# Performance work log

Measured on AMD Instinct MI355X. Metric: run time of the kernel, lower is better.

The kernel has to match this reference:

```python
import jax, jax.numpy as jnp
import numpy as np


def setup_inputs() -> dict:
    key = jax.random.key(0)
    kq, kk, kv = jax.random.split(key, 3)
    B, H, N, D = 4, 16, 2048, 64
    q = jax.random.normal(kq, (B, H, N, D), dtype=jnp.float32)
    k = jax.random.normal(kk, (B, N, D), dtype=jnp.float32)
    v = jax.random.normal(kv, (B, N, D), dtype=jnp.float32)
    return {"q": q, "k": k, "v": v}


def reference(q, k, v):
    # q: [B,H,N,D], k/v: [B,N,D] (KV shared across heads)
    scale = q.shape[-1] ** -0.5
    sim = jnp.einsum('bhid,bjd->bhij', q, k) * scale  # [B,H,N,N]
    attn = jax.nn.softmax(sim, axis=-1)
    return jnp.einsum('bhij,bjd->bhid', attn, v)  # [B,H,N,D]
```

## Files before the change

### kernel.cpp

```cpp
#include <hip/hip_runtime.h>
#include <hip/hip_bf16.h>

#define B_ 4
#define H_ 16
#define N_ 2048
#define D_ 64
#define BM 256
#define BN 64

typedef __bf16 bf16;
typedef bf16 bf16x4 __attribute__((ext_vector_type(4)));
typedef bf16 bf16x8 __attribute__((ext_vector_type(8)));
typedef float f32x2 __attribute__((ext_vector_type(2)));
typedef float f32x16 __attribute__((ext_vector_type(16)));

#define SCALE_LOG2E 0.18033688011112042f

#define GBL(p) ((const __attribute__((address_space(1))) void*)(p))
#define LDS(p) ((__attribute__((address_space(3))) void*)(p))

__global__ __launch_bounds__(256) void convert_kv(const float* __restrict__ k,
                                                  const float* __restrict__ v,
                                                  bf16* __restrict__ img) {
    const int tile = blockIdx.x >> 1;
    const int b = tile >> 5, T = tile & 31;
    const int pu = (blockIdx.x & 1) * 256 + threadIdx.x;
    const int mtks = pu >> 6;
    const int ln   = pu & 63;
    const int mt = mtks >> 2, ks = mtks & 3;
    bf16* timg = img + (size_t)tile * 8192;

    {
        const int kvr = T * 64 + mt * 32 + (ln & 31);
        const int d0  = ks * 16 + (ln >> 5) * 8;
        const float* src = k + ((size_t)b * N_ + kvr) * D_ + d0;
        float4 a = *(const float4*)src;
        float4 c = *(const float4*)(src + 4);
        bf16x8 o;
        o[0] = (bf16)a.x; o[1] = (bf16)a.y; o[2] = (bf16)a.z; o[3] = (bf16)a.w;
        o[4] = (bf16)c.x; o[5] = (bf16)c.y; o[6] = (bf16)c.z; o[7] = (bf16)c.w;
        *(bf16x8*)(timg + pu * 8) = o;
    }
    {
        const int d   = mt * 32 + (ln & 31);
        const int kv0 = T * 64 + ks * 16 + (ln >> 5) * 8;
        const float* src = v + ((size_t)b * N_ + kv0) * D_ + d;
        bf16x8 o;
        #pragma unroll
        for (int j = 0; j < 8; ++j) o[j] = (bf16)src[(size_t)j * D_];
        *(bf16x8*)(timg + 4096 + pu * 8) = o;
    }
}

static __device__ inline bf16x4 pack4(float a, float b, float c, float d) {
    bf16x4 r; r[0] = (bf16)a; r[1] = (bf16)b; r[2] = (bf16)c; r[3] = (bf16)d; return r;
}
static __device__ inline bf16x4 xor32(bf16x4 x) {
    f32x2 f = __builtin_bit_cast(f32x2, x);
    f32x2 g;
    g[0] = __shfl_xor(f[0], 32);
    g[1] = __shfl_xor(f[1], 32);
    return __builtin_bit_cast(bf16x4, g);
}

__global__ __launch_bounds__(256, 2) void attn_fwd(const float* __restrict__ q,
                                                   const bf16* __restrict__ img,
                                                   float* __restrict__ out) {
    __shared__ __align__(16) bf16 KV[2][8192];

    const int tid  = threadIdx.x;
    const int lane = tid & 63;
    const int wv   = tid >> 6;
    const int half = lane >> 5;
    const int l31  = lane & 31;

    const int bh = blockIdx.y;
    const int b  = bh >> 4;
    const int q0 = blockIdx.x * BM + wv * 64;

    const bf16* tiles = img + (size_t)b * 32 * 8192;

    bf16x8 qf[2][4];
    #pragma unroll
    for (int qn = 0; qn < 2; ++qn)
        #pragma unroll
        for (int ks = 0; ks < 4; ++ks) {
            const float* src = q + ((size_t)bh * N_ + q0 + qn * 32 + l31) * D_ + ks * 16 + half * 8;
            float4 a = *(const float4*)src;
            float4 c = *(const float4*)(src + 4);
            bf16x8 pk;
            pk[0] = (bf16)(a.x * SCALE_LOG2E); pk[1] = (bf16)(a.y * SCALE_LOG2E);
            pk[2] = (bf16)(a.z * SCALE_LOG2E); pk[3] = (bf16)(a.w * SCALE_LOG2E);
            pk[4] = (bf16)(c.x * SCALE_LOG2E); pk[5] = (bf16)(c.y * SCALE_LOG2E);
            pk[6] = (bf16)(c.z * SCALE_LOG2E); pk[7] = (bf16)(c.w * SCALE_LOG2E);
            qf[qn][ks] = pk;
        }

    f32x16 acc[2][2] = {{{}, {}}, {{}, {}}};
    float lacc[2] = {0.f, 0.f};

    auto issue_dma = [&](int it, int p) {
        const bf16* g = tiles + (size_t)it * 8192;
        #pragma unroll
        for (int j = 0; j < 4; ++j) {
            const int c = wv * 4 + j;
            __builtin_amdgcn_global_load_lds(GBL(g + c * 512 + lane * 8),
                                             LDS(&KV[p][c * 512]), 16, 0, 0);
        }
    };

    issue_dma(0, 0);

    for (int it = 0; it < N_ / BN; ++it) {
        const int p = it & 1;
        __syncthreads();
        if (it + 1 < N_ / BN) issue_dma(it + 1, p ^ 1);

        bf16x8 kf[2][4], vf[2][4];
        #pragma unroll
        for (int mt = 0; mt < 2; ++mt)
            #pragma unroll
            for (int ks = 0; ks < 4; ++ks) {
                kf[mt][ks] = *(const bf16x8*)&KV[p][((mt * 4 + ks) * 64 + lane) * 8];
                vf[mt][ks] = *(const bf16x8*)&KV[p][4096 + ((mt * 4 + ks) * 64 + lane) * 8];
            }

        #pragma unroll
        for (int qn = 0; qn < 2; ++qn) {
            f32x16 s[2] = {{}, {}};
            #pragma unroll
            for (int ks = 0; ks < 4; ++ks) {
                s[0] = __builtin_amdgcn_mfma_f32_32x32x16_bf16(kf[0][ks], qf[qn][ks], s[0], 0, 0, 0);
                s[1] = __builtin_amdgcn_mfma_f32_32x32x16_bf16(kf[1][ks], qf[qn][ks], s[1], 0, 0, 0);
            }
            #pragma unroll
            for (int mt = 0; mt < 2; ++mt) {
                float pv[16];
                #pragma unroll
                for (int r = 0; r < 16; ++r) pv[r] = __builtin_amdgcn_exp2f(s[mt][r]);
                float t0 = 0.f, t1 = 0.f;
                #pragma unroll
                for (int r = 0; r < 8; ++r) { t0 += pv[r]; t1 += pv[8 + r]; }
                lacc[qn] += t0 + t1;
                #pragma unroll
                for (int sp = 0; sp < 2; ++sp) {
                    bf16x4 lo  = pack4(pv[8 * sp + 0], pv[8 * sp + 1], pv[8 * sp + 2], pv[8 * sp + 3]);
                    bf16x4 hi  = pack4(pv[8 * sp + 4], pv[8 * sp + 5], pv[8 * sp + 6], pv[8 * sp + 7]);
                    bf16x4 xlo = xor32(lo), xhi = xor32(hi);
                    bf16x4 a0 = half ? xhi : lo;
                    bf16x4 a1 = half ? hi  : xlo;
                    bf16x8 bfrag = __builtin_shufflevector(a0, a1, 0, 1, 2, 3, 4, 5, 6, 7);
                    const int g = mt * 2 + sp;
                    acc[0][qn] = __builtin_amdgcn_mfma_f32_32x32x16_bf16(vf[0][g], bfrag, acc[0][qn], 0, 0, 0);
                    acc[1][qn] = __builtin_amdgcn_mfma_f32_32x32x16_bf16(vf[1][g], bfrag, acc[1][qn], 0, 0, 0);
                }
            }
        }
    }

    #pragma unroll
    for (int qn = 0; qn < 2; ++qn) {
        float l = lacc[qn] + __shfl_xor(lacc[qn], 32);
        float inv = 1.0f / l;
        const int qrow = q0 + qn * 32 + l31;
        float* dst = out + ((size_t)bh * N_ + qrow) * D_ + 4 * half;
        #pragma unroll
        for (int mt = 0; mt < 2; ++mt)
            #pragma unroll
            for (int rq = 0; rq < 4; ++rq) {
                float4 o;
                o.x = acc[mt][qn][4 * rq + 0] * inv;
                o.y = acc[mt][qn][4 * rq + 1] * inv;
                o.z = acc[mt][qn][4 * rq + 2] * inv;
                o.w = acc[mt][qn][4 * rq + 3] * inv;
                *(float4*)(dst + mt * 32 + 8 * rq) = o;
            }
    }
}

extern "C" void kernel_launch(void* const* d_in, const int* in_sizes, int n_in,
                              void* d_out, int out_size, void* d_ws, size_t ws_size,
                              hipStream_t stream) {
    const float* q = (const float*)d_in[0];
    const float* k = (const float*)d_in[1];
    const float* v = (const float*)d_in[2];
    float* out = (float*)d_out;

    bf16* img = (bf16*)d_ws;

    convert_kv<<<B_ * 64, 256, 0, stream>>>(k, v, img);
    dim3 grid(N_ / BM, B_ * H_);
    attn_fwd<<<grid, 256, 0, stream>>>(q, img, out);
}
```

Baseline: 155.3 us.

## Load K/V fragments directly from global into registers with double buffering

Drops the LDS staging buffer, the global_load_lds DMA and the per-iteration block barrier. Each wave now reads its K/V MFMA fragments straight from the pre-swizzled global image into two register sets, loading the next tile while computing the current one. The P-fragment cross-half exchange also changes from two shuffles to one shuffle of a selected half. This raises register pressure (two fragment sets) and makes every wave fetch the tile on its own through L2/L1 instead of sharing one LDS copy, which may hurt occupancy under launch_bounds(256,2).

```diff
diff --git a/kernel.cpp b/kernel.cpp
--- a/kernel.cpp
+++ b/kernel.cpp
@@ -15,9 +15,6 @@
 typedef float f32x16 __attribute__((ext_vector_type(16)));
 
 #define SCALE_LOG2E 0.18033688011112042f
-
-#define GBL(p) ((const __attribute__((address_space(1))) void*)(p))
-#define LDS(p) ((__attribute__((address_space(3))) void*)(p))
 
 __global__ __launch_bounds__(256) void convert_kv(const float* __restrict__ k,
                                                   const float* __restrict__ v,
@@ -55,7 +52,7 @@
 static __device__ inline bf16x4 pack4(float a, float b, float c, float d) {
     bf16x4 r; r[0] = (bf16)a; r[1] = (bf16)b; r[2] = (bf16)c; r[3] = (bf16)d; return r;
 }
-static __device__ inline bf16x4 xor32(bf16x4 x) {
+static __device__ inline bf16x4 xchg32(bf16x4 x) {
     f32x2 f = __builtin_bit_cast(f32x2, x);
     f32x2 g;
     g[0] = __shfl_xor(f[0], 32);
@@ -66,8 +63,6 @@
 __global__ __launch_bounds__(256, 2) void attn_fwd(const float* __restrict__ q,
                                                    const bf16* __restrict__ img,
                                                    float* __restrict__ out) {
-    __shared__ __align__(16) bf16 KV[2][8192];
-
     const int tid  = threadIdx.x;
     const int lane = tid & 63;
     const int wv   = tid >> 6;
@@ -78,7 +73,7 @@
     const int b  = bh >> 4;
     const int q0 = blockIdx.x * BM + wv * 64;
 
-    const bf16* tiles = img + (size_t)b * 32 * 8192;
+    const bf16* tb = img + (size_t)b * 32 * 8192 + lane * 8;
 
     bf16x8 qf[2][4];
     #pragma unroll
@@ -99,32 +94,18 @@
     f32x16 acc[2][2] = {{{}, {}}, {{}, {}}};
     float lacc[2] = {0.f, 0.f};
 
-    auto issue_dma = [&](int it, int p) {
-        const bf16* g = tiles + (size_t)it * 8192;
-        #pragma unroll
-        for (int j = 0; j < 4; ++j) {
-            const int c = wv * 4 + j;
-            __builtin_amdgcn_global_load_lds(GBL(g + c * 512 + lane * 8),
-                                             LDS(&KV[p][c * 512]), 16, 0, 0);
-        }
-    };
-
-    issue_dma(0, 0);
-
-    for (int it = 0; it < N_ / BN; ++it) {
-        const int p = it & 1;
-        __syncthreads();
-        if (it + 1 < N_ / BN) issue_dma(it + 1, p ^ 1);
-
-        bf16x8 kf[2][4], vf[2][4];
+    auto load_frags = [&](int it, bf16x8 (&kf)[2][4], bf16x8 (&vf)[2][4]) {
+        const bf16* g = tb + (size_t)it * 8192;
         #pragma unroll
         for (int mt = 0; mt < 2; ++mt)
             #pragma unroll
             for (int ks = 0; ks < 4; ++ks) {
-                kf[mt][ks] = *(const bf16x8*)&KV[p][((mt * 4 + ks) * 64 + lane) * 8];
-                vf[mt][ks] = *(const bf16x8*)&KV[p][4096 + ((mt * 4 + ks) * 64 + lane) * 8];
+                kf[mt][ks] = *(const bf16x8*)(g + (mt * 4 + ks) * 512);
+                vf[mt][ks] = *(const bf16x8*)(g + 4096 + (mt * 4 + ks) * 512);
             }
+    };
 
+    auto compute = [&](bf16x8 (&kf)[2][4], bf16x8 (&vf)[2][4]) {
         #pragma unroll
         for (int qn = 0; qn < 2; ++qn) {
             f32x16 s[2] = {{}, {}};
@@ -144,11 +125,12 @@
                 lacc[qn] += t0 + t1;
                 #pragma unroll
                 for (int sp = 0; sp < 2; ++sp) {
-                    bf16x4 lo  = pack4(pv[8 * sp + 0], pv[8 * sp + 1], pv[8 * sp + 2], pv[8 * sp + 3]);
-                    bf16x4 hi  = pack4(pv[8 * sp + 4], pv[8 * sp + 5], pv[8 * sp + 6], pv[8 * sp + 7]);
-                    bf16x4 xlo = xor32(lo), xhi = xor32(hi);
-                    bf16x4 a0 = half ? xhi : lo;
-                    bf16x4 a1 = half ? hi  : xlo;
+                    bf16x4 lo = pack4(pv[8 * sp + 0], pv[8 * sp + 1], pv[8 * sp + 2], pv[8 * sp + 3]);
+                    bf16x4 hi = pack4(pv[8 * sp + 4], pv[8 * sp + 5], pv[8 * sp + 6], pv[8 * sp + 7]);
+                    bf16x4 snd = half ? lo : hi;
+                    bf16x4 rcv = xchg32(snd);
+                    bf16x4 a0 = half ? rcv : lo;
+                    bf16x4 a1 = half ? hi  : rcv;
                     bf16x8 bfrag = __builtin_shufflevector(a0, a1, 0, 1, 2, 3, 4, 5, 6, 7);
                     const int g = mt * 2 + sp;
                     acc[0][qn] = __builtin_amdgcn_mfma_f32_32x32x16_bf16(vf[0][g], bfrag, acc[0][qn], 0, 0, 0);
@@ -156,6 +138,15 @@
                 }
             }
         }
+    };
+
+    bf16x8 kfa[2][4], vfa[2][4], kfb[2][4], vfb[2][4];
+    load_frags(0, kfa, vfa);
+    for (int it = 0; it < N_ / BN; it += 2) {
+        load_frags(it + 1, kfb, vfb);
+        compute(kfa, vfa);
+        load_frags(it + 2 < N_ / BN ? it + 2 : 0, kfa, vfa);
+        compute(kfb, vfb);
     }
 
     #pragma unroll
```

New measurement: 197.7 us. +27.3%, slower.
